# Kernel tuning notes

Hardware: AMD Instinct MI355X
Metric: run time of the kernel (lower is better)

## Reference

```python
import jax, jax.numpy as jnp
import numpy as np

FEAT, NHID, NHALF, NCLS = 256, 512, 256, 2

def _xavier(key, shape):
    fan_in, fan_out = shape[0], shape[1]
    limit = np.sqrt(6.0 / (fan_in + fan_out))
    return jax.random.uniform(key, shape, jnp.float32, -limit, limit)

def setup_inputs() -> dict:
    key = jax.random.key(0)
    ks = jax.random.split(key, 10)
    B, N = 64, 1024
    x = jax.random.normal(ks[0], (B, N, FEAT), jnp.float32)
    adj = jax.random.uniform(ks[1], (B, N, N), jnp.float32)
    adj = adj / jnp.sum(adj, axis=-1, keepdims=True)  # row-normalized (mean aggregation)
    return {
        "x": x, "adj": adj,
        "W1": _xavier(ks[2], (2 * FEAT, NHID)), "b1": jnp.zeros((NHID,), jnp.float32),
        "W2": _xavier(ks[3], (2 * NHID, NHID)), "b2": jnp.zeros((NHID,), jnp.float32),
        "W3": _xavier(ks[4], (2 * NHID, NHALF)), "b3": jnp.zeros((NHALF,), jnp.float32),
        "W4": _xavier(ks[5], (2 * NHALF, NHALF)), "b4": jnp.zeros((NHALF,), jnp.float32),
        "Wc1": _xavier(ks[6], (NHALF, NHALF)), "bc1": jnp.zeros((NHALF,), jnp.float32),
        "alpha": jnp.full((NHALF,), 0.25, jnp.float32),  # PReLU per-channel slope
        "Wc2": _xavier(ks[7], (NHALF, NCLS)), "bc2": jnp.zeros((NCLS,), jnp.float32),
    }

def _gconv(x, adj, W, b):
    # MeanAggregator: bmm(adj, x); GraphConv: relu(cat([x, agg]) @ W + b)
    agg = jnp.einsum('bnm,bmd->bnd', adj, x)
    cat = jnp.concatenate([x, agg], axis=-1)
    return jax.nn.relu(jnp.einsum('bnd,df->bnf', cat, W) + b)

def reference(x, adj, W1, b1, W2, b2, W3, b3, W4, b4, Wc1, bc1, alpha, Wc2, bc2):
    h = _gconv(x, adj, W1, b1)
    h = _gconv(h, adj, W2, b2)
    h = _gconv(h, adj, W3, b3)
    h = _gconv(h, adj, W4, b4)
    h = h.reshape(-1, h.shape[-1])  # [B*N, nhid_half]
    h = h @ Wc1 + bc1
    h = jnp.where(h > 0, h, alpha * h)  # PReLU
    logits = h @ Wc2 + bc2
    return jax.nn.log_softmax(logits, axis=-1)
```

## Files before the change

### kernel.cpp

```cpp
#include <hip/hip_runtime.h>
#include <hip/hip_bf16.h>
#include <cmath>

typedef _Float16 f16;
typedef __attribute__((ext_vector_type(4))) _Float16 f16x4;
typedef __attribute__((ext_vector_type(8))) _Float16 f16x8;
typedef __attribute__((ext_vector_type(4))) float f32x4;

__device__ inline void gload_lds16(const f16* g, f16* l) {
  __builtin_amdgcn_global_load_lds(
      (const __attribute__((address_space(1))) unsigned int*)g,
      (__attribute__((address_space(3))) unsigned int*)l, 16, 0, 0);
}

__global__ __launch_bounds__(256) void cvt_f32_f16(const float* __restrict__ in,
                                                   f16* __restrict__ out, long n) {
  long stride = (long)gridDim.x * 256 * 8;
  for (long i = ((long)blockIdx.x * 256 + threadIdx.x) * 8; i < n; i += stride) {
    float4 a = *(const float4*)(in + i);
    float4 b = *(const float4*)(in + i + 4);
    f16x8 o;
    o[0] = (f16)a.x; o[1] = (f16)a.y; o[2] = (f16)a.z; o[3] = (f16)a.w;
    o[4] = (f16)b.x; o[5] = (f16)b.y; o[6] = (f16)b.z; o[7] = (f16)b.w;
    *(f16x8*)(out + i) = o;
  }
}

__global__ __launch_bounds__(256) void transpose_cvt(const float* __restrict__ in,
                                                     f16* __restrict__ out,
                                                     int R, int C, long sIn, long sOut) {
  in  += (long)blockIdx.z * sIn;
  out += (long)blockIdx.z * sOut;
  __shared__ f16 t[32][34];
  const int tx = threadIdx.x, ty = threadIdx.y;
  const int c0 = blockIdx.x * 32, r0 = blockIdx.y * 32;
  #pragma unroll
  for (int j = 0; j < 32; j += 8)
    t[ty + j][tx] = (f16)in[(long)(r0 + ty + j) * C + (c0 + tx)];
  __syncthreads();
  #pragma unroll
  for (int j = 0; j < 32; j += 8)
    out[(long)(c0 + ty + j) * R + (r0 + tx)] = t[tx][ty + j];
}

#define MM16(AF, BF, MB)                                                        \
  do {                                                                          \
    __builtin_amdgcn_s_setprio(1);                                              \
    _Pragma("unroll") for (int m_ = 0; m_ < 4; ++m_)                            \
        _Pragma("unroll") for (int n_ = 0; n_ < 4; ++n_)                        \
            acc[(MB) + m_][n_] = __builtin_amdgcn_mfma_f32_16x16x32_f16(        \
                (AF)[m_], (BF)[n_], acc[(MB) + m_][n_], 0, 0, 0);               \
    __builtin_amdgcn_s_setprio(0);                                              \
  } while (0)

#define PHASE_SYNC()                                                            \
  do {                                                                          \
    __builtin_amdgcn_s_barrier();                                               \
    asm volatile("s_waitcnt lgkmcnt(0)" ::: "memory");                          \
    __builtin_amdgcn_sched_barrier(0);                                          \
  } while (0)

template <int ACT, bool DUAL, bool WRITE_T>
__global__ __launch_bounds__(512, 2) void gemm256(
    const f16* __restrict__ A1, int lda1,
    const f16* __restrict__ B1, int ldb1, int k1,
    const f16* __restrict__ A2, int lda2,
    const f16* __restrict__ B2, int ldb2, int k2,
    const float* __restrict__ bias, const float* __restrict__ alpha,
    f16* __restrict__ C, int ldc, f16* __restrict__ CT,
    long sA, long sB, long sC, int gxs, int gys, int nwg) {
  __shared__ __align__(16) f16 As[2][16384];
  __shared__ __align__(16) f16 Bs[2][16384];
  const int wg = blockIdx.x;
  const int lid = (wg & 7) * (nwg >> 3) + (wg >> 3);
  const int bx = lid & ((1 << gxs) - 1);
  const int by = (lid >> gxs) & ((1 << gys) - 1);
  const int z = lid >> (gxs + gys);

  const int tid = threadIdx.x;
  const f16* a1 = A1 + (long)z * sA;
  const f16* b1 = B1 + (long)z * sB;
  f16* pC = C + (long)z * sC;
  const int m0 = bx * 256, n0 = by * 256;
  const int lane = tid & 63, w = tid >> 6;
  const int wr = w >> 2, wc = w & 3;
  const int lrow = lane & 15, kg = lane >> 4;
  const int NT1 = k1 >> 6;
  const int NT = NT1 + (DUAL ? (k2 >> 6) : 0);

  const int srow = tid >> 3;
  const int cg = (tid & 7) ^ (srow & 7);
  const int ldst = (tid & 448) * 8;

  const int swz = lrow & 7;
  const int ac0 = (kg ^ swz) * 8;
  const int ac1 = ((4 + kg) ^ swz) * 8;
  const int arow = wr * 128 + lrow;
  const int brow = wc * 64 + lrow;

  f32x4 acc[8][4] = {};
  int bs = 0;

  auto stageA = [&](int kt) {
    const f16* Ab; int la, kk;
    if (!DUAL || kt < NT1) { Ab = a1; la = lda1; kk = kt << 6; }
    else { Ab = A2; la = lda2; kk = (kt - NT1) << 6; }
    const int b = kt & 1;
    #pragma unroll
    for (int j = 0; j < 4; ++j)
      gload_lds16(Ab + (long)(m0 + srow + j * 64) * la + kk + cg * 8,
                  &As[b][j * 4096 + ldst]);
  };
  auto stageB = [&](int kt) {
    const f16* Bb; int lb, kk;
    if (!DUAL || kt < NT1) { Bb = b1; lb = ldb1; kk = kt << 6; }
    else { Bb = B2; lb = ldb2; kk = (kt - NT1) << 6; }
    const int b = kt & 1;
    #pragma unroll
    for (int j = 0; j < 4; ++j)
      gload_lds16(Bb + (long)(n0 + srow + j * 64) * lb + kk + cg * 8,
                  &Bs[b][j * 4096 + ldst]);
  };
  auto rdB = [&](f16x8* bf, int ac) {
    #pragma unroll
    for (int n = 0; n < 4; ++n)
      bf[n] = *(const f16x8*)&Bs[bs][(brow + n * 16) * 64 + ac];
  };
  auto rdA = [&](f16x8* af, int mo, int ac) {
    #pragma unroll
    for (int m = 0; m < 4; ++m)
      af[m] = *(const f16x8*)&As[bs][(arow + mo + m * 16) * 64 + ac];
  };

  stageA(0); stageB(0); stageB(1);
  asm volatile("s_waitcnt vmcnt(4)" ::: "memory");
  __builtin_amdgcn_s_barrier();

  for (int t = 0; t < NT; ++t) {
    bs = t & 1;
    f16x8 bf0[4], bf1[4], af[4];
    if (t + 1 < NT) stageA(t + 1);
    rdB(bf0, ac0); rdA(af, 0, ac0);
    PHASE_SYNC();
    MM16(af, bf0, 0);
    __builtin_amdgcn_s_barrier();
    rdB(bf1, ac1); rdA(af, 0, ac1);
    PHASE_SYNC();
    MM16(af, bf1, 0);
    __builtin_amdgcn_s_barrier();
    if (t + 2 < NT) stageB(t + 2);
    rdA(af, 64, ac0);
    PHASE_SYNC();
    MM16(af, bf0, 4);
    __builtin_amdgcn_s_barrier();
    rdA(af, 64, ac1);
    PHASE_SYNC();
    MM16(af, bf1, 4);
    __builtin_amdgcn_s_barrier();
    if (t + 1 < NT) {
      if (t + 2 < NT)
        asm volatile("s_waitcnt vmcnt(4)" ::: "memory");
      else
        asm volatile("s_waitcnt vmcnt(0)" ::: "memory");
      __builtin_amdgcn_s_barrier();
    }
  }

  #pragma unroll
  for (int n = 0; n < 4; ++n) {
    const int gn = n0 + wc * 64 + n * 16 + lrow;
    const float bv = bias ? bias[gn] : 0.0f;
    const float av = (ACT == 2) ? alpha[gn] : 0.0f;
    #pragma unroll
    for (int m = 0; m < 8; ++m) {
      const int rg0 = m0 + wr * 128 + m * 16 + kg * 4;
      f16 tv[4];
      #pragma unroll
      for (int r = 0; r < 4; ++r) {
        float v = acc[m][n][r] + bv;
        if (ACT == 1) v = fmaxf(v, 0.0f);
        if (ACT == 2) v = (v > 0.0f) ? v : av * v;
        const f16 h = (f16)v;
        tv[r] = h;
        pC[(long)(rg0 + r) * ldc + gn] = h;
      }
      if (WRITE_T) {
        const int b = rg0 >> 10, node = rg0 & 1023;
        f16x4 pk;
        pk[0] = tv[0]; pk[1] = tv[1]; pk[2] = tv[2]; pk[3] = tv[3];
        *(f16x4*)&CT[((long)b * ldc + gn) * 1024 + node] = pk;
      }
    }
  }
}

__global__ __launch_bounds__(256) void logits_lsm(const f16* __restrict__ hc,
                                                  const float* __restrict__ Wc2,
                                                  const float* __restrict__ bc2,
                                                  float* __restrict__ out) {
  __shared__ float w[512];
  __shared__ float bb[2];
  const int t = threadIdx.x;
  w[t] = Wc2[t];
  w[t + 256] = Wc2[t + 256];
  if (t < 2) bb[t] = bc2[t];
  __syncthreads();
  const long row = (long)blockIdx.x * 256 + t;
  const f16* hr = hc + row * 256;
  float l0 = 0.f, l1 = 0.f;
  #pragma unroll 4
  for (int d0 = 0; d0 < 256; d0 += 8) {
    f16x8 v = *(const f16x8*)(hr + d0);
    #pragma unroll
    for (int j = 0; j < 8; ++j) {
      const float p = (float)v[j];
      l0 += p * w[(d0 + j) * 2];
      l1 += p * w[(d0 + j) * 2 + 1];
    }
  }
  l0 += bb[0];
  l1 += bb[1];
  const float mx = fmaxf(l0, l1);
  const float lse = mx + logf(expf(l0 - mx) + expf(l1 - mx));
  out[row * 2] = l0 - lse;
  out[row * 2 + 1] = l1 - lse;
}

extern "C" void kernel_launch(void* const* d_in, const int* in_sizes, int n_in,
                              void* d_out, int out_size, void* d_ws, size_t ws_size,
                              hipStream_t stream) {
  const float* x     = (const float*)d_in[0];
  const float* adj   = (const float*)d_in[1];
  const float* W1    = (const float*)d_in[2];
  const float* b1    = (const float*)d_in[3];
  const float* W2    = (const float*)d_in[4];
  const float* b2    = (const float*)d_in[5];
  const float* W3    = (const float*)d_in[6];
  const float* b3    = (const float*)d_in[7];
  const float* W4    = (const float*)d_in[8];
  const float* b4    = (const float*)d_in[9];
  const float* Wc1   = (const float*)d_in[10];
  const float* bc1   = (const float*)d_in[11];
  const float* alpha = (const float*)d_in[12];
  const float* Wc2   = (const float*)d_in[13];
  const float* bc2   = (const float*)d_in[14];
  float* out = (float*)d_out;

  char* ws = (char*)d_ws;
  f16* adjB = (f16*)(ws + 0L);
  f16* xN   = (f16*)(ws + 134217728L);
  f16* xT   = (f16*)(ws + 167772160L);
  f16* agg  = (f16*)(ws + 201326592L);
  f16* hAN  = (f16*)(ws + 268435456L);
  f16* hAT  = (f16*)(ws + 335544320L);
  f16* hBN  = (f16*)(ws + 402653184L);
  f16* hBT  = (f16*)(ws + 469762048L);
  f16* WT1  = (f16*)(ws + 536870912L);
  f16* WT2  = (f16*)(ws + 537395200L);
  f16* WT3  = (f16*)(ws + 538443776L);
  f16* WT4  = (f16*)(ws + 538968064L);
  f16* WTc1 = (f16*)(ws + 539230208L);
  if (ws_size < (size_t)539361280L) return;

  const dim3 tb(32, 8, 1);

  cvt_f32_f16<<<2048, 256, 0, stream>>>(adj, adjB, 64L * 1024 * 1024);
  cvt_f32_f16<<<1024, 256, 0, stream>>>(x, xN, 64L * 1024 * 256);
  transpose_cvt<<<dim3(8, 32, 64), tb, 0, stream>>>(x, xT, 1024, 256, 1024L * 256, 256L * 1024);
  transpose_cvt<<<dim3(16, 16, 1), tb, 0, stream>>>(W1, WT1, 512, 512, 0, 0);
  transpose_cvt<<<dim3(16, 32, 1), tb, 0, stream>>>(W2, WT2, 1024, 512, 0, 0);
  transpose_cvt<<<dim3(8, 32, 1), tb, 0, stream>>>(W3, WT3, 1024, 256, 0, 0);
  transpose_cvt<<<dim3(8, 16, 1), tb, 0, stream>>>(W4, WT4, 512, 256, 0, 0);
  transpose_cvt<<<dim3(8, 8, 1), tb, 0, stream>>>(Wc1, WTc1, 256, 256, 0, 0);

  gemm256<0, false, false><<<256, 512, 0, stream>>>(
      adjB, 1024, xT, 1024, 1024,
      nullptr, 0, nullptr, 0, 0,
      nullptr, nullptr, agg, 256, nullptr,
      1024L * 1024, 256L * 1024, 1024L * 256, 2, 0, 256);
  gemm256<1, true, true><<<512, 512, 0, stream>>>(
      xN, 256, WT1, 512, 256,
      agg, 256, WT1 + 256, 512, 256,
      b1, nullptr, hAN, 512, hAT, 0, 0, 0, 8, 1, 512);

  gemm256<0, false, false><<<512, 512, 0, stream>>>(
      adjB, 1024, hAT, 1024, 1024,
      nullptr, 0, nullptr, 0, 0,
      nullptr, nullptr, agg, 512, nullptr,
      1024L * 1024, 512L * 1024, 1024L * 512, 2, 1, 512);
  gemm256<1, true, true><<<512, 512, 0, stream>>>(
      hAN, 512, WT2, 1024, 512,
      agg, 512, WT2 + 512, 1024, 512,
      b2, nullptr, hBN, 512, hBT, 0, 0, 0, 8, 1, 512);

  gemm256<0, false, false><<<512, 512, 0, stream>>>(
      adjB, 1024, hBT, 1024, 1024,
      nullptr, 0, nullptr, 0, 0,
      nullptr, nullptr, agg, 512, nullptr,
      1024L * 1024, 512L * 1024, 1024L * 512, 2, 1, 512);
  gemm256<1, true, true><<<256, 512, 0, stream>>>(
      hBN, 512, WT3, 1024, 512,
      agg, 512, WT3 + 512, 1024, 512,
      b3, nullptr, hAN, 256, hAT, 0, 0, 0, 8, 0, 256);

  gemm256<0, false, false><<<256, 512, 0, stream>>>(
      adjB, 1024, hAT, 1024, 1024,
      nullptr, 0, nullptr, 0, 0,
      nullptr, nullptr, agg, 256, nullptr,
      1024L * 1024, 256L * 1024, 1024L * 256, 2, 0, 256);
  gemm256<1, true, false><<<256, 512, 0, stream>>>(
      hAN, 256, WT4, 512, 256,
      agg, 256, WT4 + 256, 512, 256,
      b4, nullptr, hBN, 256, nullptr, 0, 0, 0, 8, 0, 256);

  gemm256<2, false, false><<<256, 512, 0, stream>>>(
      hBN, 256, WTc1, 256, 256,
      nullptr, 0, nullptr, 0, 0,
      bc1, alpha, hAN, 256, nullptr, 0, 0, 0, 8, 0, 256);

  logits_lsm<<<256, 256, 0, stream>>>(hAN, Wc2, bc2, out);
}
```

Before: 1.134 ms.

## Triple-buffer A tiles, swap tile ordering, fuse x convert and transpose

```diff
diff --git a/kernel.cpp b/kernel.cpp
--- a/kernel.cpp
+++ b/kernel.cpp
@@ -43,6 +43,28 @@
     out[(long)(c0 + ty + j) * R + (r0 + tx)] = t[tx][ty + j];
 }
 
+__global__ __launch_bounds__(256) void xprep(const float* __restrict__ in,
+                                             f16* __restrict__ outN,
+                                             f16* __restrict__ outT,
+                                             int R, int C, long sIn) {
+  in   += (long)blockIdx.z * sIn;
+  outN += (long)blockIdx.z * sIn;
+  outT += (long)blockIdx.z * sIn;
+  __shared__ f16 t[32][34];
+  const int tx = threadIdx.x, ty = threadIdx.y;
+  const int c0 = blockIdx.x * 32, r0 = blockIdx.y * 32;
+  #pragma unroll
+  for (int j = 0; j < 32; j += 8) {
+    const f16 v = (f16)in[(long)(r0 + ty + j) * C + (c0 + tx)];
+    t[ty + j][tx] = v;
+    outN[(long)(r0 + ty + j) * C + (c0 + tx)] = v;
+  }
+  __syncthreads();
+  #pragma unroll
+  for (int j = 0; j < 32; j += 8)
+    outT[(long)(c0 + ty + j) * R + (r0 + tx)] = t[tx][ty + j];
+}
+
 #define MM16(AF, BF, MB)                                                        \
   do {                                                                          \
     __builtin_amdgcn_s_setprio(1);                                              \
@@ -69,12 +91,12 @@
     const float* __restrict__ bias, const float* __restrict__ alpha,
     f16* __restrict__ C, int ldc, f16* __restrict__ CT,
     long sA, long sB, long sC, int gxs, int gys, int nwg) {
-  __shared__ __align__(16) f16 As[2][16384];
+  __shared__ __align__(16) f16 As[3][16384];
   __shared__ __align__(16) f16 Bs[2][16384];
   const int wg = blockIdx.x;
   const int lid = (wg & 7) * (nwg >> 3) + (wg >> 3);
-  const int bx = lid & ((1 << gxs) - 1);
-  const int by = (lid >> gxs) & ((1 << gys) - 1);
+  const int by = lid & ((1 << gys) - 1);
+  const int bx = (lid >> gys) & ((1 << gxs) - 1);
   const int z = lid >> (gxs + gys);
 
   const int tid = threadIdx.x;
@@ -99,17 +121,15 @@
   const int brow = wc * 64 + lrow;
 
   f32x4 acc[8][4] = {};
-  int bs = 0;
-
-  auto stageA = [&](int kt) {
+
+  auto stageA = [&](int kt, int buf) {
     const f16* Ab; int la, kk;
     if (!DUAL || kt < NT1) { Ab = a1; la = lda1; kk = kt << 6; }
     else { Ab = A2; la = lda2; kk = (kt - NT1) << 6; }
-    const int b = kt & 1;
     #pragma unroll
     for (int j = 0; j < 4; ++j)
       gload_lds16(Ab + (long)(m0 + srow + j * 64) * la + kk + cg * 8,
-                  &As[b][j * 4096 + ldst]);
+                  &As[buf][j * 4096 + ldst]);
   };
   auto stageB = [&](int kt) {
     const f16* Bb; int lb, kk;
@@ -121,49 +141,56 @@
       gload_lds16(Bb + (long)(n0 + srow + j * 64) * lb + kk + cg * 8,
                   &Bs[b][j * 4096 + ldst]);
   };
-  auto rdB = [&](f16x8* bf, int ac) {
+
+  stageA(0, 0); stageB(0); stageA(1, 1); stageB(1);
+  asm volatile("s_waitcnt vmcnt(8)" ::: "memory");
+  __builtin_amdgcn_s_barrier();
+
+  int abuf = 0;
+  for (int t = 0; t < NT; ++t) {
+    const int bbuf = t & 1;
+    const int anext = (abuf + 2 >= 3) ? abuf - 1 : abuf + 2;
+    f16x8 bf0[4], bf1[4], af[4];
+    if (t + 2 < NT) stageA(t + 2, anext);
     #pragma unroll
     for (int n = 0; n < 4; ++n)
-      bf[n] = *(const f16x8*)&Bs[bs][(brow + n * 16) * 64 + ac];
-  };
-  auto rdA = [&](f16x8* af, int mo, int ac) {
+      bf0[n] = *(const f16x8*)&Bs[bbuf][(brow + n * 16) * 64 + ac0];
     #pragma unroll
     for (int m = 0; m < 4; ++m)
-      af[m] = *(const f16x8*)&As[bs][(arow + mo + m * 16) * 64 + ac];
-  };
-
-  stageA(0); stageB(0); stageB(1);
-  asm volatile("s_waitcnt vmcnt(4)" ::: "memory");
-  __builtin_amdgcn_s_barrier();
-
-  for (int t = 0; t < NT; ++t) {
-    bs = t & 1;
-    f16x8 bf0[4], bf1[4], af[4];
-    if (t + 1 < NT) stageA(t + 1);
-    rdB(bf0, ac0); rdA(af, 0, ac0);
+      af[m] = *(const f16x8*)&As[abuf][(arow + m * 16) * 64 + ac0];
     PHASE_SYNC();
     MM16(af, bf0, 0);
     __builtin_amdgcn_s_barrier();
-    rdB(bf1, ac1); rdA(af, 0, ac1);
+    #pragma unroll
+    for (int n = 0; n < 4; ++n)
+      bf1[n] = *(const f16x8*)&Bs[bbuf][(brow + n * 16) * 64 + ac1];
+    #pragma unroll
+    for (int m = 0; m < 4; ++m)
+      af[m] = *(const f16x8*)&As[abuf][(arow + m * 16) * 64 + ac1];
     PHASE_SYNC();
     MM16(af, bf1, 0);
     __builtin_amdgcn_s_barrier();
     if (t + 2 < NT) stageB(t + 2);
-    rdA(af, 64, ac0);
+    #pragma unroll
+    for (int m = 0; m < 4; ++m)
+      af[m] = *(const f16x8*)&As[abuf][(arow + 64 + m * 16) * 64 + ac0];
     PHASE_SYNC();
     MM16(af, bf0, 4);
     __builtin_amdgcn_s_barrier();
-    rdA(af, 64, ac1);
+    #pragma unroll
+    for (int m = 0; m < 4; ++m)
+      af[m] = *(const f16x8*)&As[abuf][(arow + 64 + m * 16) * 64 + ac1];
     PHASE_SYNC();
     MM16(af, bf1, 4);
     __builtin_amdgcn_s_barrier();
     if (t + 1 < NT) {
       if (t + 2 < NT)
-        asm volatile("s_waitcnt vmcnt(4)" ::: "memory");
+        asm volatile("s_waitcnt vmcnt(8)" ::: "memory");
       else
         asm volatile("s_waitcnt vmcnt(0)" ::: "memory");
       __builtin_amdgcn_s_barrier();
     }
+    abuf = (abuf + 1 >= 3) ? 0 : abuf + 1;
   }
 
   #pragma unroll
@@ -265,8 +292,7 @@
   const dim3 tb(32, 8, 1);
 
   cvt_f32_f16<<<2048, 256, 0, stream>>>(adj, adjB, 64L * 1024 * 1024);
-  cvt_f32_f16<<<1024, 256, 0, stream>>>(x, xN, 64L * 1024 * 256);
-  transpose_cvt<<<dim3(8, 32, 64), tb, 0, stream>>>(x, xT, 1024, 256, 1024L * 256, 256L * 1024);
+  xprep<<<dim3(8, 32, 64), tb, 0, stream>>>(x, xN, xT, 1024, 256, 1024L * 256);
   transpose_cvt<<<dim3(16, 16, 1), tb, 0, stream>>>(W1, WT1, 512, 512, 0, 0);
   transpose_cvt<<<dim3(16, 32, 1), tb, 0, stream>>>(W2, WT2, 1024, 512, 0, 0);
   transpose_cvt<<<dim3(8, 32, 1), tb, 0, stream>>>(W3, WT3, 1024, 256, 0, 0);
```

Measured after the change: 1.121 ms. Within noise of the previous version (-1.1%).
